# Kernel optimization log

Measured on AMD Instinct MI355X. Metric: run time of the kernel, lower is better.

## Reference

```python
import jax, jax.numpy as jnp
import numpy as np

UNITS = 1024
INPUT_DIM = 512
BATCH = 2048

def setup_inputs() -> dict:
    key = jax.random.key(0)
    k1, k2, k3, k4 = jax.random.split(key, 4)
    return {
        "inputs": jax.random.normal(k1, (BATCH, INPUT_DIM), dtype=jnp.float32),
        "h_tm1": jax.random.normal(k2, (BATCH, UNITS), dtype=jnp.float32),
        "c_tm1": jax.random.normal(k3, (BATCH, UNITS), dtype=jnp.float32),
        # keras 'random_normal' initializer: stddev 0.05
        "kernel": jax.random.normal(k4, (UNITS + INPUT_DIM, 4 * UNITS), dtype=jnp.float32) * 0.05,
    }

def reference(inputs, h_tm1, c_tm1, kernel):
    # z = concat([h, x]) @ kernel ; kernel rows: [units (h-block); input_dim (x-block)]
    z = jnp.concatenate([h_tm1, inputs], axis=-1) @ kernel  # [B, 4*units]
    z0, z1, z2, z3 = jnp.split(z, 4, axis=-1)
    i = jax.nn.sigmoid(z0)
    f = jax.nn.sigmoid(z1)
    c_tilde = jnp.tanh(z2)
    o = jax.nn.sigmoid(z3)
    c = f * c_tm1 + i * c_tilde
    h = o * jnp.tanh(c)
    return (h, c)
```

## Files before the change

kernel.cpp:

```cpp
#include <hip/hip_runtime.h>
#include <hip/hip_bf16.h>
#include <stdint.h>

#define UNITS 1024
#define IDIM  512
#define BATCH 2048
#define KTOT  1536
#define NGATE 4096
#define BK    64

typedef short bf16x8 __attribute__((ext_vector_type(8)));
typedef float f32x4  __attribute__((ext_vector_type(4)));

#define AS3(p) ((__attribute__((address_space(3))) void*)(p))
#define AS1(p) ((const __attribute__((address_space(1))) void*)(p))

union P8 { bf16x8 v; __hip_bfloat16 e[8]; };

#define NBLK_A 1536
#define NBLK_T 3072

__global__ __launch_bounds__(256) void prep(
    const float* __restrict__ x, const float* __restrict__ h,
    const float* __restrict__ W,
    __hip_bfloat16* __restrict__ A, __hip_bfloat16* __restrict__ Wt) {
  __shared__ float tile[32][65];
  const int tid = threadIdx.x;
  if (blockIdx.x < NBLK_A) {
    const int id = blockIdx.x * 256 + tid;
    const int r = id / (KTOT / 8);
    const int k = (id % (KTOT / 8)) * 8;
    const float* src = (k < UNITS) ? h + (size_t)r * UNITS + k
                                   : x + (size_t)r * IDIM + (k - UNITS);
    const float4 v0 = ((const float4*)src)[0];
    const float4 v1 = ((const float4*)src)[1];
    P8 o;
    o.e[0] = __float2bfloat16(v0.x); o.e[1] = __float2bfloat16(v0.y);
    o.e[2] = __float2bfloat16(v0.z); o.e[3] = __float2bfloat16(v0.w);
    o.e[4] = __float2bfloat16(v1.x); o.e[5] = __float2bfloat16(v1.y);
    o.e[6] = __float2bfloat16(v1.z); o.e[7] = __float2bfloat16(v1.w);
    *(bf16x8*)(A + (size_t)r * KTOT + k) = o.v;
  } else {
    const int b  = blockIdx.x - NBLK_A;
    const int kb = b >> 7;
    const int nb = b & 127;
    const int k0 = kb * 64, n0 = nb * 32;
    const int n4 = (tid & 7) * 4;
    const int kk = tid >> 3;
#pragma unroll
    for (int rr = 0; rr < 64; rr += 32) {
      const float4 v = *(const float4*)(W + (size_t)(k0 + kk + rr) * NGATE + n0 + n4);
      tile[n4 + 0][kk + rr] = v.x; tile[n4 + 1][kk + rr] = v.y;
      tile[n4 + 2][kk + rr] = v.z; tile[n4 + 3][kk + rr] = v.w;
    }
    __syncthreads();
    const int n  = tid >> 3;
    const int k8 = (tid & 7) * 8;
    P8 o;
#pragma unroll
    for (int j = 0; j < 8; ++j) o.e[j] = __float2bfloat16(tile[n][k8 + j]);
    *(bf16x8*)(Wt + (size_t)(n0 + n) * KTOT + k0 + k8) = o.v;
  }
}

__global__ __launch_bounds__(256, 4) void lstm_gemm(
    const __hip_bfloat16* __restrict__ A,
    const __hip_bfloat16* __restrict__ Wt,
    const float* __restrict__ c_tm1,
    float* __restrict__ out) {
  __shared__ __attribute__((aligned(128))) char lds[24576];

  const int tid  = threadIdx.x;
  const int w    = tid >> 6;
  const int lane = tid & 63;
  const int quad = lane >> 4;
  const int m16  = lane & 15;
  const int wr   = w >> 1;
  const int wc   = w & 1;

  const int bi = blockIdx.x;
  const int ub = ((bi & 7) << 2) | ((bi >> 3) & 3);
  const int mb = bi >> 5;
  const int m0 = mb * 64;
  const int u0 = ub * 32;

  const __hip_bfloat16* ptr[6];
  int dstoff[6];
#pragma unroll
  for (int s = 0; s < 6; ++s) {
    const int q = s * 4 + w;
    if (q < 8) {
      const int ci  = q * 64 + lane;
      const int row = ci >> 3;
      const int k8  = (ci & 7) ^ (row & 7);
      ptr[s]    = A + (size_t)(m0 + row) * KTOT + k8 * 8;
      dstoff[s] = q * 1024;
    } else {
      const int ci   = (q - 8) * 64 + lane;
      const int vr   = ci >> 3;
      const int k8   = (ci & 7) ^ (vr & 7);
      const int wrow = ((vr >> 5) << 10) + u0 + (vr & 31);
      ptr[s]    = Wt + (size_t)wrow * KTOT + k8 * 8;
      dstoff[s] = 8192 + (q - 8) * 1024;
    }
  }

  f32x4 acc[2][4];
#pragma unroll
  for (int i = 0; i < 2; ++i)
#pragma unroll
    for (int g = 0; g < 4; ++g) {
      f32x4 z = {0.f, 0.f, 0.f, 0.f};
      acc[i][g] = z;
    }

  for (int kt = 0; kt < KTOT; kt += BK) {
#pragma unroll
    for (int s = 0; s < 6; ++s) {
      __builtin_amdgcn_global_load_lds(AS1(ptr[s]), AS3(lds + dstoff[s]), 16, 0, 0);
      ptr[s] += BK;
    }
    __syncthreads();

#pragma unroll
    for (int t = 0; t < 2; ++t) {
      bf16x8 a[2], b[4];
#pragma unroll
      for (int i = 0; i < 2; ++i) {
        const int row  = 32 * wr + 16 * i + m16;
        const int slot = (t * 4 + quad) ^ (row & 7);
        a[i] = *(const bf16x8*)(lds + (row * 8 + slot) * 16);
      }
#pragma unroll
      for (int g = 0; g < 4; ++g) {
        const int vr   = g * 32 + wc * 16 + m16;
        const int slot = (t * 4 + quad) ^ (vr & 7);
        b[g] = *(const bf16x8*)(lds + 8192 + (vr * 8 + slot) * 16);
      }
#pragma unroll
      for (int g = 0; g < 4; ++g)
#pragma unroll
        for (int i = 0; i < 2; ++i)
          acc[i][g] = __builtin_amdgcn_mfma_f32_16x16x32_bf16(a[i], b[g], acc[i][g], 0, 0, 0);
    }
    __syncthreads();
  }

#pragma unroll
  for (int i = 0; i < 2; ++i)
#pragma unroll
    for (int reg = 0; reg < 4; ++reg) {
      const int r = m0 + 32 * wr + 16 * i + quad * 4 + reg;
      const int u = u0 + wc * 16 + m16;
      const float z0 = acc[i][0][reg];
      const float z1 = acc[i][1][reg];
      const float z2 = acc[i][2][reg];
      const float z3 = acc[i][3][reg];
      const float ig = 1.f / (1.f + __expf(-z0));
      const float fg = 1.f / (1.f + __expf(-z1));
      const float ct = 1.f - 2.f / (__expf(2.f * z2) + 1.f);
      const float og = 1.f / (1.f + __expf(-z3));
      const float cc = fg * c_tm1[(size_t)r * UNITS + u] + ig * ct;
      const float hh = og * (1.f - 2.f / (__expf(2.f * cc) + 1.f));
      out[(size_t)r * UNITS + u] = hh;
      out[(size_t)BATCH * UNITS + (size_t)r * UNITS + u] = cc;
    }
}

__global__ __launch_bounds__(256) void lstm_naive(
    const float* __restrict__ x, const float* __restrict__ h,
    const float* __restrict__ c_tm1, const float* __restrict__ W,
    float* __restrict__ out) {
  int idx = blockIdx.x * 256 + threadIdx.x;
  int r = idx / UNITS;
  int u = idx % UNITS;
  float z[4] = {0.f, 0.f, 0.f, 0.f};
  for (int k = 0; k < KTOT; ++k) {
    float a = (k < UNITS) ? h[(size_t)r * UNITS + k] : x[(size_t)r * IDIM + k - UNITS];
#pragma unroll
    for (int g = 0; g < 4; ++g)
      z[g] += a * W[(size_t)k * NGATE + g * UNITS + u];
  }
  float ig = 1.f / (1.f + __expf(-z[0]));
  float fg = 1.f / (1.f + __expf(-z[1]));
  float ct = 1.f - 2.f / (__expf(2.f * z[2]) + 1.f);
  float og = 1.f / (1.f + __expf(-z[3]));
  float cc = fg * c_tm1[(size_t)r * UNITS + u] + ig * ct;
  float hh = og * (1.f - 2.f / (__expf(2.f * cc) + 1.f));
  out[(size_t)r * UNITS + u] = hh;
  out[(size_t)BATCH * UNITS + (size_t)r * UNITS + u] = cc;
}

extern "C" void kernel_launch(void* const* d_in, const int* in_sizes, int n_in,
                              void* d_out, int out_size, void* d_ws, size_t ws_size,
                              hipStream_t stream) {
  const float* x = (const float*)d_in[0];
  const float* h = (const float*)d_in[1];
  const float* c = (const float*)d_in[2];
  const float* W = (const float*)d_in[3];
  float* out = (float*)d_out;

  const size_t needA  = (size_t)BATCH * KTOT * sizeof(__hip_bfloat16);
  const size_t needWt = (size_t)NGATE * KTOT * sizeof(__hip_bfloat16);
  if (ws_size < needA + needWt) {
    hipLaunchKernelGGL(lstm_naive, dim3((BATCH * UNITS) / 256), dim3(256), 0, stream,
                       x, h, c, W, out);
    return;
  }

  __hip_bfloat16* A  = (__hip_bfloat16*)d_ws;
  __hip_bfloat16* Wt = (__hip_bfloat16*)((char*)d_ws + needA);

  hipLaunchKernelGGL(prep, dim3(NBLK_A + NBLK_T), dim3(256), 0, stream, x, h, W, A, Wt);
  hipLaunchKernelGGL(lstm_gemm, dim3(1024), dim3(256), 0, stream, A, Wt, c, out);
}
```

Before: 126.1 us.

## Double-buffer A tiles in LDS, load W directly to registers, enlarge M tile

The GEMM block tile grows from 64 to 128 rows, so each wave computes a 64x32 slice with 16 accumulators and half as many blocks are launched. The A tile is now double-buffered in LDS so the next K-slice is fetched while the current one is computed, removing one barrier per iteration. The weight fragments are loaded straight from global memory into registers, also double-buffered, instead of being staged through LDS. This raises register pressure and lowers occupancy (launch bounds drop from 4 to 2), and the per-lane global reads of W may be less coalesced than the old LDS path.

Result: slower. 151.7 us (+20.3%).

```diff
diff --git a/kernel.cpp b/kernel.cpp
--- a/kernel.cpp
+++ b/kernel.cpp
@@ -8,6 +8,7 @@
 #define KTOT  1536
 #define NGATE 4096
 #define BK    64
+#define NITER (KTOT / BK)
 
 typedef short bf16x8 __attribute__((ext_vector_type(8)));
 typedef float f32x4  __attribute__((ext_vector_type(4)));
@@ -63,12 +64,12 @@
   }
 }
 
-__global__ __launch_bounds__(256, 4) void lstm_gemm(
+__global__ __launch_bounds__(256, 2) void lstm_gemm(
     const __hip_bfloat16* __restrict__ A,
     const __hip_bfloat16* __restrict__ Wt,
     const float* __restrict__ c_tm1,
     float* __restrict__ out) {
-  __shared__ __attribute__((aligned(128))) char lds[24576];
+  __shared__ __attribute__((aligned(128))) char lds[2 * 16384];
 
   const int tid  = threadIdx.x;
   const int w    = tid >> 6;
@@ -76,82 +77,92 @@
   const int quad = lane >> 4;
   const int m16  = lane & 15;
   const int wr   = w >> 1;
-  const int wc   = w & 1;
-
-  const int bi = blockIdx.x;
-  const int ub = ((bi & 7) << 2) | ((bi >> 3) & 3);
-  const int mb = bi >> 5;
-  const int m0 = mb * 64;
+  const int wu   = w & 1;
+
+  const int mb = blockIdx.x >> 5;
+  const int ub = blockIdx.x & 31;
+  const int m0 = mb * 128;
   const int u0 = ub * 32;
 
-  const __hip_bfloat16* ptr[6];
-  int dstoff[6];
-#pragma unroll
-  for (int s = 0; s < 6; ++s) {
-    const int q = s * 4 + w;
-    if (q < 8) {
-      const int ci  = q * 64 + lane;
-      const int row = ci >> 3;
-      const int k8  = (ci & 7) ^ (row & 7);
-      ptr[s]    = A + (size_t)(m0 + row) * KTOT + k8 * 8;
-      dstoff[s] = q * 1024;
-    } else {
-      const int ci   = (q - 8) * 64 + lane;
-      const int vr   = ci >> 3;
-      const int k8   = (ci & 7) ^ (vr & 7);
-      const int wrow = ((vr >> 5) << 10) + u0 + (vr & 31);
-      ptr[s]    = Wt + (size_t)wrow * KTOT + k8 * 8;
-      dstoff[s] = 8192 + (q - 8) * 1024;
-    }
-  }
-
-  f32x4 acc[2][4];
-#pragma unroll
-  for (int i = 0; i < 2; ++i)
+  const __hip_bfloat16* aptr[4];
+  int adst[4];
+#pragma unroll
+  for (int s = 0; s < 4; ++s) {
+    const int q   = s * 4 + w;
+    const int ci  = q * 64 + lane;
+    const int row = ci >> 3;
+    const int k8  = (ci & 7) ^ (row & 7);
+    aptr[s] = A + (size_t)(m0 + row) * KTOT + k8 * 8;
+    adst[s] = q * 1024;
+  }
+
+  const __hip_bfloat16* bp[4];
+#pragma unroll
+  for (int g = 0; g < 4; ++g)
+    bp[g] = Wt + (size_t)((g << 10) + u0 + wu * 16 + m16) * KTOT + quad * 8;
+
+  f32x4 acc[4][4];
+#pragma unroll
+  for (int i = 0; i < 4; ++i)
 #pragma unroll
     for (int g = 0; g < 4; ++g) {
       f32x4 z = {0.f, 0.f, 0.f, 0.f};
       acc[i][g] = z;
     }
 
-  for (int kt = 0; kt < KTOT; kt += BK) {
-#pragma unroll
-    for (int s = 0; s < 6; ++s) {
-      __builtin_amdgcn_global_load_lds(AS1(ptr[s]), AS3(lds + dstoff[s]), 16, 0, 0);
-      ptr[s] += BK;
+  bf16x8 breg[2][4][2];
+
+#pragma unroll
+  for (int s = 0; s < 4; ++s)
+    __builtin_amdgcn_global_load_lds(AS1(aptr[s]), AS3(lds + adst[s]), 16, 0, 0);
+#pragma unroll
+  for (int g = 0; g < 4; ++g)
+#pragma unroll
+    for (int t = 0; t < 2; ++t)
+      breg[0][g][t] = *(const bf16x8*)(bp[g] + t * 32);
+  __syncthreads();
+
+#pragma unroll 2
+  for (int it = 0; it < NITER; ++it) {
+    const int cur = it & 1;
+    const int nxt = cur ^ 1;
+    if (it < NITER - 1) {
+      const int koff = (it + 1) * BK;
+#pragma unroll
+      for (int s = 0; s < 4; ++s)
+        __builtin_amdgcn_global_load_lds(AS1(aptr[s] + koff),
+                                         AS3(lds + nxt * 16384 + adst[s]), 16, 0, 0);
+#pragma unroll
+      for (int g = 0; g < 4; ++g)
+#pragma unroll
+        for (int t = 0; t < 2; ++t)
+          breg[nxt][g][t] = *(const bf16x8*)(bp[g] + koff + t * 32);
+    }
+#pragma unroll
+    for (int t = 0; t < 2; ++t) {
+      bf16x8 a[4];
+#pragma unroll
+      for (int i = 0; i < 4; ++i) {
+        const int row  = wr * 64 + i * 16 + m16;
+        const int slot = (t * 4 + quad) ^ (row & 7);
+        a[i] = *(const bf16x8*)(lds + cur * 16384 + (row * 8 + slot) * 16);
+      }
+#pragma unroll
+      for (int g = 0; g < 4; ++g)
+#pragma unroll
+        for (int i = 0; i < 4; ++i)
+          acc[i][g] = __builtin_amdgcn_mfma_f32_16x16x32_bf16(a[i], breg[cur][g][t],
+                                                              acc[i][g], 0, 0, 0);
     }
     __syncthreads();
-
-#pragma unroll
-    for (int t = 0; t < 2; ++t) {
-      bf16x8 a[2], b[4];
-#pragma unroll
-      for (int i = 0; i < 2; ++i) {
-        const int row  = 32 * wr + 16 * i + m16;
-        const int slot = (t * 4 + quad) ^ (row & 7);
-        a[i] = *(const bf16x8*)(lds + (row * 8 + slot) * 16);
-      }
-#pragma unroll
-      for (int g = 0; g < 4; ++g) {
-        const int vr   = g * 32 + wc * 16 + m16;
-        const int slot = (t * 4 + quad) ^ (vr & 7);
-        b[g] = *(const bf16x8*)(lds + 8192 + (vr * 8 + slot) * 16);
-      }
-#pragma unroll
-      for (int g = 0; g < 4; ++g)
-#pragma unroll
-        for (int i = 0; i < 2; ++i)
-          acc[i][g] = __builtin_amdgcn_mfma_f32_16x16x32_bf16(a[i], b[g], acc[i][g], 0, 0, 0);
-    }
-    __syncthreads();
-  }
-
-#pragma unroll
-  for (int i = 0; i < 2; ++i)
+  }
+
+  const int u = u0 + wu * 16 + m16;
+#pragma unroll
+  for (int i = 0; i < 4; ++i)
 #pragma unroll
     for (int reg = 0; reg < 4; ++reg) {
-      const int r = m0 + 32 * wr + 16 * i + quad * 4 + reg;
-      const int u = u0 + wc * 16 + m16;
+      const int r = m0 + wr * 64 + i * 16 + quad * 4 + reg;
       const float z0 = acc[i][0][reg];
       const float z1 = acc[i][1][reg];
       const float z2 = acc[i][2][reg];
@@ -212,5 +223,5 @@
   __hip_bfloat16* Wt = (__hip_bfloat16*)((char*)d_ws + needA);
 
   hipLaunchKernelGGL(prep, dim3(NBLK_A + NBLK_T), dim3(256), 0, stream, x, h, W, A, Wt);
-  hipLaunchKernelGGL(lstm_gemm, dim3(1024), dim3(256), 0, stream, A, Wt, c, out);
-}
+  hipLaunchKernelGGL(lstm_gemm, dim3(512), dim3(256), 0, stream, A, Wt, c, out);
+}
```
